# Optimization experiments

Measured on AMD Instinct MI355X. Metric: run time of the kernel, lower is better.

## Reference

```python
import jax, jax.numpy as jnp
import numpy as np

B, S, H, A, E = 64, 1024, 1024, 512, 512


def setup_inputs() -> dict:
    key = jax.random.key(0)
    ks = jax.random.split(key, 13)
    sc = 0.02
    return {
        "inputs": jax.random.normal(ks[0], (B, E), jnp.float32),
        "states": jax.random.normal(ks[1], (B, H), jnp.float32),
        "encoded": jax.random.normal(ks[2], (B, S, H), jnp.float32),
        "W_enc": jax.random.normal(ks[3], (H, A), jnp.float32) * sc,
        "b_enc": jax.random.normal(ks[4], (A,), jnp.float32) * sc,
        "W_dec": jax.random.normal(ks[5], (H, A), jnp.float32) * sc,
        "b_dec": jax.random.normal(ks[6], (A,), jnp.float32) * sc,
        "w_out": jax.random.normal(ks[7], (A,), jnp.float32) * sc,
        "b_out": jax.random.normal(ks[8], (1,), jnp.float32) * sc,
        "W_ih": jax.random.normal(ks[9], (E + H, 3 * H), jnp.float32) * sc,
        "b_ih": jax.random.normal(ks[10], (3 * H,), jnp.float32) * sc,
        "W_hh": jax.random.normal(ks[11], (H, 3 * H), jnp.float32) * sc,
        "b_hh": jax.random.normal(ks[12], (3 * H,), jnp.float32) * sc,
    }


def reference(inputs, states, encoded, W_enc, b_enc, W_dec, b_dec, w_out, b_out,
              W_ih, b_ih, W_hh, b_hh):
    # setup_memory: project encoder states once  [B,S,H] @ [H,A] -> [B,S,A]
    enc_proj = jnp.einsum('bsh,ha->bsa', encoded, W_enc) + b_enc
    # Bahdanau additive attention
    dec_proj = states @ W_dec + b_dec                       # [B,A]
    scores = jnp.einsum('bsa,a->bs', jnp.tanh(enc_proj + dec_proj[:, None, :]), w_out) + b_out[0]
    weights = jax.nn.softmax(scores, axis=1)                # [B,S]
    attention = jnp.einsum('bs,bsh->bh', weights, encoded)  # [B,H]
    x = jnp.concatenate([inputs, attention], axis=-1)       # [B,E+H]
    # GRUCell (PyTorch gate order r, z, n)
    gi = x @ W_ih + b_ih                                    # [B,3H]
    gh = states @ W_hh + b_hh                               # [B,3H]
    i_r, i_z, i_n = jnp.split(gi, 3, axis=-1)
    h_r, h_z, h_n = jnp.split(gh, 3, axis=-1)
    r = jax.nn.sigmoid(i_r + h_r)
    z = jax.nn.sigmoid(i_z + h_z)
    n = jnp.tanh(i_n + r * h_n)
    h_new = (1.0 - z) * n + z * states
    return h_new
```

## Files before the change

### kernel.cpp

```cpp
#include <hip/hip_runtime.h>
#include <hip/hip_bf16.h>


typedef __attribute__((ext_vector_type(8))) __bf16 bf16x8;
typedef __attribute__((ext_vector_type(4))) __bf16 bf16x4;
typedef __attribute__((ext_vector_type(4))) float f32x4;

__device__ __forceinline__ float fast_tanh(float x) {
  float xa = fminf(fmaxf(x, -15.f), 15.f);
  float e = __expf(2.f * xa);
  return (e - 1.f) / (e + 1.f);
}

#define GLOAD16(G, L)                                                              \
  __builtin_amdgcn_global_load_lds(                                                \
      (const __attribute__((address_space(1))) unsigned int*)(const void*)(G),     \
      (__attribute__((address_space(3))) unsigned int*)(void*)(L), 16, 0, 0)

__global__ __launch_bounds__(256) void wenc_t_kernel(const float* __restrict__ W,
                                                     __bf16* __restrict__ Wt) {
  __shared__ float tile[32][33];
  int k0 = blockIdx.x * 32, a0 = blockIdx.y * 32;
  int tid = threadIdx.x;
  int r = tid >> 3, c4 = (tid & 7) * 4;
  f32x4 v = *(const f32x4*)(W + (long)(k0 + r) * 512 + a0 + c4);
  tile[r][c4 + 0] = v.x; tile[r][c4 + 1] = v.y;
  tile[r][c4 + 2] = v.z; tile[r][c4 + 3] = v.w;
  __syncthreads();
  int a = tid >> 3, k4 = (tid & 7) * 4;
  bf16x4 o = { (__bf16)tile[k4 + 0][a], (__bf16)tile[k4 + 1][a],
               (__bf16)tile[k4 + 2][a], (__bf16)tile[k4 + 3][a] };
  *(bf16x4*)(Wt + (long)(a0 + a) * 1024 + k0 + k4) = o;
}

__global__ __launch_bounds__(256) void dec_proj_kernel(
    const float* __restrict__ states, const float* __restrict__ W_dec,
    const float* __restrict__ b_enc, const float* __restrict__ b_dec,
    float* __restrict__ addv) {
  int b = blockIdx.x, tid = threadIdx.x;
  int a = blockIdx.y * 256 + tid;
  __shared__ float sl[1024];
  for (int i = tid; i < 1024; i += 256) sl[i] = states[b * 1024 + i];
  __syncthreads();
  float c0 = 0.f, c1 = 0.f, c2 = 0.f, c3 = 0.f;
#pragma unroll 4
  for (int i = 0; i < 256; ++i) {
    c0 += sl[i]         * W_dec[(i)        * 512 + a];
    c1 += sl[i + 256]   * W_dec[(i + 256)  * 512 + a];
    c2 += sl[i + 512]   * W_dec[(i + 512)  * 512 + a];
    c3 += sl[i + 768]   * W_dec[(i + 768)  * 512 + a];
  }
  addv[b * 512 + a] = c0 + c1 + c2 + c3 + b_enc[a] + b_dec[a];
}

__global__ __launch_bounds__(256, 3) void enc_score_kernel(
    const float* __restrict__ encoded,
    const __bf16* __restrict__ Wt,
    const float* __restrict__ addv,
    const float* __restrict__ w_out,
    float* __restrict__ psc)
{
  __shared__ __attribute__((aligned(16))) char smem[50176];
  float* red = (float*)(smem + 49152);

  const int d = blockIdx.x;
  const int xcd = d & 7;
  const int slot = d >> 3;
  const int bn = slot & 3;
  const int bm = ((slot >> 2) << 3) | xcd;

  const int tid = threadIdx.x;
  const int lane = tid & 63;
  const int wid = tid >> 6;
  const int wr = wid >> 1;
  const int wc = wid & 1;
  const int lr = lane & 15;
  const int lkb = lane >> 4;

  const long row0 = (long)bm * 128;
  const int col0 = bn * 128;

  const int aslot = (tid & 7) ^ ((tid >> 3) & 7);
  const char* gA = (const char*)encoded + (row0 + (tid >> 3)) * 4096 + (aslot << 4);
  const int bslot = (tid & 3) ^ ((tid >> 3) & 3);
  const char* gB = (const char*)Wt + (long)(col0 + (tid >> 2)) * 2048 + (bslot << 4);
  const int ldsW = wid * 1024;

  const int aoff0 = ((2 * lkb) ^ (lr & 7)) << 4;
  const int aoff1 = ((2 * lkb + 1) ^ (lr & 7)) << 4;
  const int boff = (lkb ^ ((lr >> 1) & 3)) << 4;
  const int aRowB = (wr * 64 + lr) * 128;
  const int bColB = (wc * 64 + lr) * 64;

  f32x4 acc[4][4];
#pragma unroll
  for (int m = 0; m < 4; ++m)
#pragma unroll
    for (int n = 0; n < 4; ++n) acc[m][n] = (f32x4){0.f, 0.f, 0.f, 0.f};

#define STAGE(BUF, KT) do {                                                        \
    _Pragma("unroll") for (int _i = 0; _i < 4; ++_i)                               \
      GLOAD16(gA + (long)_i * 131072 + (KT) * 128,                                 \
              smem + (BUF) * 16384 + _i * 4096 + ldsW);                            \
    _Pragma("unroll") for (int _i = 0; _i < 2; ++_i)                               \
      GLOAD16(gB + (long)_i * 131072 + (KT) * 64,                                  \
              smem + 32768 + (BUF) * 8192 + _i * 4096 + ldsW);                     \
  } while (0)

#define COMPUTE(BUF) do {                                                          \
    const char* _Ab = smem + (BUF) * 16384;                                        \
    const char* _Bb = smem + 32768 + (BUF) * 8192;                                 \
    bf16x8 _af[4], _bv[4];                                                         \
    _Pragma("unroll") for (int _m = 0; _m < 4; ++_m) {                             \
      f32x4 _lo = *(const f32x4*)(_Ab + aRowB + _m * 2048 + aoff0);                \
      f32x4 _hi = *(const f32x4*)(_Ab + aRowB + _m * 2048 + aoff1);                \
      _Pragma("unroll") for (int _j = 0; _j < 4; ++_j) {                           \
        _af[_m][_j] = (__bf16)_lo[_j]; _af[_m][4 + _j] = (__bf16)_hi[_j];          \
      }                                                                            \
    }                                                                              \
    _Pragma("unroll") for (int _n = 0; _n < 4; ++_n)                               \
      _bv[_n] = *(const bf16x8*)(_Bb + bColB + _n * 1024 + boff);                  \
    _Pragma("unroll") for (int _m = 0; _m < 4; ++_m)                               \
      _Pragma("unroll") for (int _n = 0; _n < 4; ++_n)                             \
        acc[_m][_n] =                                                              \
            __builtin_amdgcn_mfma_f32_16x16x32_bf16(_af[_m], _bv[_n], acc[_m][_n], 0, 0, 0); \
  } while (0)

  STAGE(0, 0);
  __syncthreads();
  int buf = 0;
  for (int kt = 0; kt < 32; ++kt) {
    if (kt < 31) STAGE(buf ^ 1, kt + 1);
    COMPUTE(buf);
    __syncthreads();
    buf ^= 1;
  }

#undef STAGE
#undef COMPUTE

  const int b = bm >> 3;
  const float* addvb = addv + b * 512;
  float rowsum[4][4];
#pragma unroll
  for (int m = 0; m < 4; ++m)
#pragma unroll
    for (int reg = 0; reg < 4; ++reg) rowsum[m][reg] = 0.f;

#pragma unroll
  for (int m = 0; m < 4; ++m) {
#pragma unroll
    for (int n = 0; n < 4; ++n) {
      int col = col0 + wc * 64 + n * 16 + lr;
      float av = addvb[col];
      float wo = w_out[col];
#pragma unroll
      for (int reg = 0; reg < 4; ++reg)
        rowsum[m][reg] += fast_tanh(acc[m][n][reg] + av) * wo;
    }
  }
#pragma unroll
  for (int m = 0; m < 4; ++m)
#pragma unroll
    for (int reg = 0; reg < 4; ++reg) {
      float v = rowsum[m][reg];
      v += __shfl_xor(v, 1, 64);
      v += __shfl_xor(v, 2, 64);
      v += __shfl_xor(v, 4, 64);
      v += __shfl_xor(v, 8, 64);
      rowsum[m][reg] = v;
    }
  if (lr == 0) {
#pragma unroll
    for (int m = 0; m < 4; ++m)
#pragma unroll
      for (int reg = 0; reg < 4; ++reg)
        red[(wr * 64 + m * 16 + lkb * 4 + reg) * 2 + wc] = rowsum[m][reg];
  }
  __syncthreads();
  if (tid < 128)
    psc[(long)bn * 65536 + row0 + tid] = red[tid * 2] + red[tid * 2 + 1];
}

__global__ __launch_bounds__(256) void softmax_kernel(const float* __restrict__ psc,
                                                      float* __restrict__ wts) {
  int b = blockIdx.x, tid = threadIdx.x;
  __shared__ float sred[8];
  float sc[4];
  float mx = -1e30f;
#pragma unroll
  for (int i = 0; i < 4; ++i) {
    long r = (long)b * 1024 + tid + i * 256;
    sc[i] = psc[r] + psc[65536 + r] + psc[2 * 65536 + r] + psc[3 * 65536 + r];
    mx = fmaxf(mx, sc[i]);
  }
  for (int off = 1; off < 64; off <<= 1) mx = fmaxf(mx, __shfl_xor(mx, off, 64));
  if ((tid & 63) == 0) sred[tid >> 6] = mx;
  __syncthreads();
  mx = fmaxf(fmaxf(sred[0], sred[1]), fmaxf(sred[2], sred[3]));
  float e[4], sum = 0.f;
#pragma unroll
  for (int i = 0; i < 4; ++i) {
    e[i] = __expf(sc[i] - mx);
    sum += e[i];
  }
  for (int off = 1; off < 64; off <<= 1) sum += __shfl_xor(sum, off, 64);
  if ((tid & 63) == 0) sred[4 + (tid >> 6)] = sum;
  __syncthreads();
  sum = sred[4] + sred[5] + sred[6] + sred[7];
  float inv = 1.f / sum;
#pragma unroll
  for (int i = 0; i < 4; ++i) wts[(long)b * 1024 + tid + i * 256] = e[i] * inv;
}

__global__ __launch_bounds__(256) void att_part_kernel(const float* __restrict__ encoded,
                                                       const float* __restrict__ wts,
                                                       float* __restrict__ attp) {
  int chunk = blockIdx.x;
  int b = blockIdx.y;
  int tid = threadIdx.x;
  f32x4 a0 = (f32x4){0.f, 0.f, 0.f, 0.f};
  f32x4 a1 = a0, a2 = a0, a3 = a0;
  const float* base = encoded + ((long)b * 1024 + chunk * 64) * 1024 + tid * 4;
  const float* w = wts + b * 1024 + chunk * 64;
#pragma unroll 4
  for (int s = 0; s < 64; s += 4) {
    f32x4 v0 = *(const f32x4*)(base + (long)(s + 0) * 1024);
    f32x4 v1 = *(const f32x4*)(base + (long)(s + 1) * 1024);
    f32x4 v2 = *(const f32x4*)(base + (long)(s + 2) * 1024);
    f32x4 v3 = *(const f32x4*)(base + (long)(s + 3) * 1024);
    a0 += v0 * w[s]; a1 += v1 * w[s + 1]; a2 += v2 * w[s + 2]; a3 += v3 * w[s + 3];
  }
  *(f32x4*)(attp + ((long)(b * 16 + chunk)) * 1024 + tid * 4) = (a0 + a1) + (a2 + a3);
}

__global__ __launch_bounds__(256) void xcat_kernel(const float* __restrict__ inputs,
                                                   const float* __restrict__ attp,
                                                   float* __restrict__ xcat) {
  int b = blockIdx.y;
  int k = blockIdx.x * 256 + threadIdx.x;
  float v;
  if (k < 512) {
    v = inputs[b * 512 + k];
  } else {
    int h = k - 512;
    v = 0.f;
#pragma unroll
    for (int c = 0; c < 16; ++c) v += attp[((long)(b * 16 + c)) * 1024 + h];
  }
  xcat[(long)b * 1536 + k] = v;
}

__global__ __launch_bounds__(512) void gru_gemv_kernel(
    const float* __restrict__ xcat, const float* __restrict__ states,
    const float* __restrict__ W_ih, const float* __restrict__ b_ih,
    const float* __restrict__ W_hh, const float* __restrict__ b_hh,
    float* __restrict__ gi, float* __restrict__ gh) {
  __shared__ float sx[12288];
  const int dd = blockIdx.x;
  const int xcd = dd & 7;
  const int n = dd >> 3;
  const int cgrp = xcd + 8 * (n >> 3);
  const int bg = n & 7;
  const int tid = threadIdx.x;
  const int lcol = tid & 255;
  const int bsel = (tid >> 8) * 4;

  if (cgrp < 12) {
    const int col = cgrp * 256 + lcol;
    const float* xb = xcat + (long)bg * 8 * 1536;
    for (int i = tid; i < 3072; i += 512) ((f32x4*)sx)[i] = ((const f32x4*)xb)[i];
    __syncthreads();
    float a0 = b_ih[col], a1 = a0, a2 = a0, a3 = a0;
    const float* x0 = sx + (bsel + 0) * 1536;
    const float* x1 = sx + (bsel + 1) * 1536;
    const float* x2 = sx + (bsel + 2) * 1536;
    const float* x3 = sx + (bsel + 3) * 1536;
    for (int k = 0; k < 1536; k += 4) {
      f32x4 v0 = *(const f32x4*)(x0 + k);
      f32x4 v1 = *(const f32x4*)(x1 + k);
      f32x4 v2 = *(const f32x4*)(x2 + k);
      f32x4 v3 = *(const f32x4*)(x3 + k);
#pragma unroll
      for (int j = 0; j < 4; ++j) {
        float w = W_ih[(long)(k + j) * 3072 + col];
        a0 += v0[j] * w; a1 += v1[j] * w; a2 += v2[j] * w; a3 += v3[j] * w;
      }
    }
    long o = (long)(bg * 8 + bsel) * 3072 + col;
    gi[o] = a0; gi[o + 3072] = a1; gi[o + 6144] = a2; gi[o + 9216] = a3;
  } else {
    const int col = (cgrp - 12) * 256 + lcol;
    const float* sb = states + (long)bg * 8 * 1024;
    for (int i = tid; i < 2048; i += 512) ((f32x4*)sx)[i] = ((const f32x4*)sb)[i];
    __syncthreads();
    float a0 = b_hh[col], a1 = a0, a2 = a0, a3 = a0;
    const float* x0 = sx + (bsel + 0) * 1024;
    const float* x1 = sx + (bsel + 1) * 1024;
    const float* x2 = sx + (bsel + 2) * 1024;
    const float* x3 = sx + (bsel + 3) * 1024;
    for (int k = 0; k < 1024; k += 4) {
      f32x4 v0 = *(const f32x4*)(x0 + k);
      f32x4 v1 = *(const f32x4*)(x1 + k);
      f32x4 v2 = *(const f32x4*)(x2 + k);
      f32x4 v3 = *(const f32x4*)(x3 + k);
#pragma unroll
      for (int j = 0; j < 4; ++j) {
        float w = W_hh[(long)(k + j) * 3072 + col];
        a0 += v0[j] * w; a1 += v1[j] * w; a2 += v2[j] * w; a3 += v3[j] * w;
      }
    }
    long o = (long)(bg * 8 + bsel) * 3072 + col;
    gh[o] = a0; gh[o + 3072] = a1; gh[o + 6144] = a2; gh[o + 9216] = a3;
  }
}

__global__ __launch_bounds__(256) void gate_kernel(const float* __restrict__ gi,
                                                   const float* __restrict__ gh,
                                                   const float* __restrict__ states,
                                                   float* __restrict__ out) {
  int b = blockIdx.y;
  int j = blockIdx.x * 256 + threadIdx.x;
  long o = (long)b * 3072;
  float ir = gi[o + j], hr = gh[o + j];
  float iz = gi[o + 1024 + j], hz = gh[o + 1024 + j];
  float in_ = gi[o + 2048 + j], hn = gh[o + 2048 + j];
  float r = 1.f / (1.f + __expf(-(ir + hr)));
  float z = 1.f / (1.f + __expf(-(iz + hz)));
  float n = fast_tanh(in_ + r * hn);
  out[(long)b * 1024 + j] = (1.f - z) * n + z * states[(long)b * 1024 + j];
}

extern "C" void kernel_launch(void* const* d_in, const int* in_sizes, int n_in,
                              void* d_out, int out_size, void* d_ws, size_t ws_size,
                              hipStream_t stream) {
  const float* inputs  = (const float*)d_in[0];
  const float* states  = (const float*)d_in[1];
  const float* encoded = (const float*)d_in[2];
  const float* W_enc   = (const float*)d_in[3];
  const float* b_enc   = (const float*)d_in[4];
  const float* W_dec   = (const float*)d_in[5];
  const float* b_dec   = (const float*)d_in[6];
  const float* w_out   = (const float*)d_in[7];
  const float* W_ih    = (const float*)d_in[9];
  const float* b_ih    = (const float*)d_in[10];
  const float* W_hh    = (const float*)d_in[11];
  const float* b_hh    = (const float*)d_in[12];
  float* out = (float*)d_out;
  float* ws = (float*)d_ws;

  float* addv = ws;
  float* psc  = ws + 32768;
  float* wts  = ws + 294912;
  float* attp = ws + 360448;
  float* xcat = ws + 1409024;
  float* gi   = ws + 1507328;
  float* gh   = ws + 1703936;
  __bf16* Wt  = (__bf16*)(ws + 1900544);

  wenc_t_kernel<<<dim3(32, 16), 256, 0, stream>>>(W_enc, Wt);

  dim3 gA(64, 2);
  dec_proj_kernel<<<gA, 256, 0, stream>>>(states, W_dec, b_enc, b_dec, addv);

  enc_score_kernel<<<2048, 256, 0, stream>>>(encoded, Wt, addv, w_out, psc);

  softmax_kernel<<<64, 256, 0, stream>>>(psc, wts);

  dim3 gD(16, 64);
  att_part_kernel<<<gD, 256, 0, stream>>>(encoded, wts, attp);

  dim3 gE(6, 64);
  xcat_kernel<<<gE, 256, 0, stream>>>(inputs, attp, xcat);

  gru_gemv_kernel<<<192, 512, 0, stream>>>(xcat, states, W_ih, b_ih, W_hh, b_hh, gi, gh);

  dim3 gG(4, 64);
  gate_kernel<<<gG, 256, 0, stream>>>(gi, gh, states, out);
}
```

Baseline: 333.6 us.

## Pre-convert encoder states to bf16 in workspace for score GEMM and attention

Adds a pass that converts the whole fp32 encoded tensor to bf16 in workspace, used only when the workspace is large enough. The score GEMM then loads bf16 tiles straight into LDS with a smaller footprint and no in-loop fp32-to-bf16 conversion, and the attention-weighted sum reads the bf16 copy. The aim is to cut conversion ALU work and LDS traffic in the MFMA loop, and halve the bytes read by both consumers. In exchange, the extra pass reads the full fp32 tensor and writes a bf16 copy, so total memory traffic may rise. Attention values also lose precision. The original fp32 kernels remain as a fallback.

```diff
diff --git a/kernel.cpp b/kernel.cpp
--- a/kernel.cpp
+++ b/kernel.cpp
@@ -16,6 +16,23 @@
   __builtin_amdgcn_global_load_lds(                                                \
       (const __attribute__((address_space(1))) unsigned int*)(const void*)(G),     \
       (__attribute__((address_space(3))) unsigned int*)(void*)(L), 16, 0, 0)
+
+__global__ __launch_bounds__(256) void conv_kernel(const float* __restrict__ in,
+                                                   __bf16* __restrict__ out, long n16) {
+  long stride = (long)gridDim.x * 256;
+  for (long i = (long)blockIdx.x * 256 + threadIdx.x; i < n16; i += stride) {
+    const f32x4* p = (const f32x4*)(in + i * 16);
+    f32x4 v0 = p[0], v1 = p[1], v2 = p[2], v3 = p[3];
+    bf16x8 o0, o1;
+#pragma unroll
+    for (int j = 0; j < 4; ++j) {
+      o0[j] = (__bf16)v0[j]; o0[4 + j] = (__bf16)v1[j];
+      o1[j] = (__bf16)v2[j]; o1[4 + j] = (__bf16)v3[j];
+    }
+    *(bf16x8*)(out + i * 16) = o0;
+    *(bf16x8*)(out + i * 16 + 8) = o1;
+  }
+}
 
 __global__ __launch_bounds__(256) void wenc_t_kernel(const float* __restrict__ W,
                                                      __bf16* __restrict__ Wt) {
@@ -54,14 +71,14 @@
 }
 
 __global__ __launch_bounds__(256, 3) void enc_score_kernel(
-    const float* __restrict__ encoded,
+    const __bf16* __restrict__ encB,
     const __bf16* __restrict__ Wt,
     const float* __restrict__ addv,
     const float* __restrict__ w_out,
     float* __restrict__ psc)
 {
-  __shared__ __attribute__((aligned(16))) char smem[50176];
-  float* red = (float*)(smem + 49152);
+  __shared__ __attribute__((aligned(16))) char smem[33792];
+  float* red = (float*)(smem + 32768);
 
   const int d = blockIdx.x;
   const int xcd = d & 7;
@@ -80,24 +97,132 @@
   const long row0 = (long)bm * 128;
   const int col0 = bn * 128;
 
+  const int srow = tid >> 2;
+  const int sk8 = (tid & 3) ^ ((srow >> 1) & 3);
+  const __bf16* gA = encB + (row0 + srow) * 1024 + sk8 * 8;
+  const __bf16* gB = Wt + (long)(col0 + srow) * 1024 + sk8 * 8;
+  const int ldsW = wid * 1024;
+
+  const int foff = (lkb ^ ((lr >> 1) & 3)) << 4;
+  const int aRowB = (wr * 64 + lr) * 64;
+  const int bColB = (wc * 64 + lr) * 64;
+
+  f32x4 acc[4][4];
+#pragma unroll
+  for (int m = 0; m < 4; ++m)
+#pragma unroll
+    for (int n = 0; n < 4; ++n) acc[m][n] = (f32x4){0.f, 0.f, 0.f, 0.f};
+
+#define STAGE(BUF, KT) do {                                                        \
+    GLOAD16(gA + (KT) * 32,           smem + (BUF) * 8192 + ldsW);                 \
+    GLOAD16(gA + (KT) * 32 + 65536,   smem + (BUF) * 8192 + 4096 + ldsW);          \
+    GLOAD16(gB + (KT) * 32,           smem + 16384 + (BUF) * 8192 + ldsW);         \
+    GLOAD16(gB + (KT) * 32 + 65536,   smem + 16384 + (BUF) * 8192 + 4096 + ldsW);  \
+  } while (0)
+
+#define COMPUTE(BUF) do {                                                          \
+    const char* _Ab = smem + (BUF) * 8192;                                         \
+    const char* _Bb = smem + 16384 + (BUF) * 8192;                                 \
+    bf16x8 _af[4], _bv[4];                                                         \
+    _Pragma("unroll") for (int _m = 0; _m < 4; ++_m)                               \
+      _af[_m] = *(const bf16x8*)(_Ab + aRowB + _m * 1024 + foff);                  \
+    _Pragma("unroll") for (int _n = 0; _n < 4; ++_n)                               \
+      _bv[_n] = *(const bf16x8*)(_Bb + bColB + _n * 1024 + foff);                  \
+    _Pragma("unroll") for (int _m = 0; _m < 4; ++_m)                               \
+      _Pragma("unroll") for (int _n = 0; _n < 4; ++_n)                             \
+        acc[_m][_n] =                                                              \
+            __builtin_amdgcn_mfma_f32_16x16x32_bf16(_af[_m], _bv[_n], acc[_m][_n], 0, 0, 0); \
+  } while (0)
+
+  STAGE(0, 0);
+  __syncthreads();
+  int buf = 0;
+  for (int kt = 0; kt < 32; ++kt) {
+    if (kt < 31) STAGE(buf ^ 1, kt + 1);
+    COMPUTE(buf);
+    __syncthreads();
+    buf ^= 1;
+  }
+
+#undef STAGE
+#undef COMPUTE
+
+  const int b = bm >> 3;
+  const float* addvb = addv + b * 512;
+  float rowsum[4][4];
+#pragma unroll
+  for (int m = 0; m < 4; ++m)
+#pragma unroll
+    for (int reg = 0; reg < 4; ++reg) rowsum[m][reg] = 0.f;
+
+#pragma unroll
+  for (int m = 0; m < 4; ++m) {
+#pragma unroll
+    for (int n = 0; n < 4; ++n) {
+      int col = col0 + wc * 64 + n * 16 + lr;
+      float av = addvb[col];
+      float wo = w_out[col];
+#pragma unroll
+      for (int reg = 0; reg < 4; ++reg)
+        rowsum[m][reg] += fast_tanh(acc[m][n][reg] + av) * wo;
+    }
+  }
+#pragma unroll
+  for (int m = 0; m < 4; ++m)
+#pragma unroll
+    for (int reg = 0; reg < 4; ++reg) {
+      float v = rowsum[m][reg];
+      v += __shfl_xor(v, 1, 64);
+      v += __shfl_xor(v, 2, 64);
+      v += __shfl_xor(v, 4, 64);
+      v += __shfl_xor(v, 8, 64);
+      rowsum[m][reg] = v;
+    }
+  if (lr == 0) {
+#pragma unroll
+    for (int m = 0; m < 4; ++m)
+#pragma unroll
+      for (int reg = 0; reg < 4; ++reg)
+        red[(wr * 64 + m * 16 + lkb * 4 + reg) * 2 + wc] = rowsum[m][reg];
+  }
+  __syncthreads();
+  if (tid < 128)
+    psc[(long)bn * 65536 + row0 + tid] = red[tid * 2] + red[tid * 2 + 1];
+}
+
+__global__ __launch_bounds__(256, 3) void enc_score_f32_kernel(
+    const float* __restrict__ encoded, const __bf16* __restrict__ Wt,
+    const float* __restrict__ addv, const float* __restrict__ w_out,
+    float* __restrict__ psc) {
+  __shared__ __attribute__((aligned(16))) char smem[50176];
+  float* red = (float*)(smem + 49152);
+  const int d = blockIdx.x;
+  const int xcd = d & 7;
+  const int slot = d >> 3;
+  const int bn = slot & 3;
+  const int bm = ((slot >> 2) << 3) | xcd;
+  const int tid = threadIdx.x;
+  const int lane = tid & 63;
+  const int wid = tid >> 6;
+  const int wr = wid >> 1, wc = wid & 1;
+  const int lr = lane & 15, lkb = lane >> 4;
+  const long row0 = (long)bm * 128;
+  const int col0 = bn * 128;
   const int aslot = (tid & 7) ^ ((tid >> 3) & 7);
   const char* gA = (const char*)encoded + (row0 + (tid >> 3)) * 4096 + (aslot << 4);
   const int bslot = (tid & 3) ^ ((tid >> 3) & 3);
   const char* gB = (const char*)Wt + (long)(col0 + (tid >> 2)) * 2048 + (bslot << 4);
   const int ldsW = wid * 1024;
-
   const int aoff0 = ((2 * lkb) ^ (lr & 7)) << 4;
   const int aoff1 = ((2 * lkb + 1) ^ (lr & 7)) << 4;
   const int boff = (lkb ^ ((lr >> 1) & 3)) << 4;
   const int aRowB = (wr * 64 + lr) * 128;
   const int bColB = (wc * 64 + lr) * 64;
-
   f32x4 acc[4][4];
 #pragma unroll
   for (int m = 0; m < 4; ++m)
 #pragma unroll
     for (int n = 0; n < 4; ++n) acc[m][n] = (f32x4){0.f, 0.f, 0.f, 0.f};
-
 #define STAGE(BUF, KT) do {                                                        \
     _Pragma("unroll") for (int _i = 0; _i < 4; ++_i)                               \
       GLOAD16(gA + (long)_i * 131072 + (KT) * 128,                                 \
@@ -106,7 +231,6 @@
       GLOAD16(gB + (long)_i * 131072 + (KT) * 64,                                  \
               smem + 32768 + (BUF) * 8192 + _i * 4096 + ldsW);                     \
   } while (0)
-
 #define COMPUTE(BUF) do {                                                          \
     const char* _Ab = smem + (BUF) * 16384;                                        \
     const char* _Bb = smem + 32768 + (BUF) * 8192;                                 \
@@ -125,7 +249,6 @@
         acc[_m][_n] =                                                              \
             __builtin_amdgcn_mfma_f32_16x16x32_bf16(_af[_m], _bv[_n], acc[_m][_n], 0, 0, 0); \
   } while (0)
-
   STAGE(0, 0);
   __syncthreads();
   int buf = 0;
@@ -135,10 +258,8 @@
     __syncthreads();
     buf ^= 1;
   }
-
 #undef STAGE
 #undef COMPUTE
-
   const int b = bm >> 3;
   const float* addvb = addv + b * 512;
   float rowsum[4][4];
@@ -146,7 +267,6 @@
   for (int m = 0; m < 4; ++m)
 #pragma unroll
     for (int reg = 0; reg < 4; ++reg) rowsum[m][reg] = 0.f;
-
 #pragma unroll
   for (int m = 0; m < 4; ++m) {
 #pragma unroll
@@ -211,6 +331,33 @@
   float inv = 1.f / sum;
 #pragma unroll
   for (int i = 0; i < 4; ++i) wts[(long)b * 1024 + tid + i * 256] = e[i] * inv;
+}
+
+__global__ __launch_bounds__(128) void att_part_bf16_kernel(const __bf16* __restrict__ encB,
+                                                            const float* __restrict__ wts,
+                                                            float* __restrict__ attp) {
+  int chunk = blockIdx.x;
+  int b = blockIdx.y;
+  int tid = threadIdx.x;
+  const __bf16* base = encB + ((long)b * 1024 + chunk * 64) * 1024 + tid * 8;
+  const float* w = wts + b * 1024 + chunk * 64;
+  float a0[8], a1[8];
+#pragma unroll
+  for (int j = 0; j < 8; ++j) { a0[j] = 0.f; a1[j] = 0.f; }
+#pragma unroll 4
+  for (int s = 0; s < 64; s += 2) {
+    bf16x8 v0 = *(const bf16x8*)(base + (long)s * 1024);
+    bf16x8 v1 = *(const bf16x8*)(base + (long)(s + 1) * 1024);
+    float w0 = w[s], w1 = w[s + 1];
+#pragma unroll
+    for (int j = 0; j < 8; ++j) {
+      a0[j] += (float)v0[j] * w0;
+      a1[j] += (float)v1[j] * w1;
+    }
+  }
+  float* o = attp + ((long)(b * 16 + chunk)) * 1024 + tid * 8;
+#pragma unroll
+  for (int j = 0; j < 8; ++j) o[j] = a0[j] + a1[j];
 }
 
 __global__ __launch_bounds__(256) void att_part_kernel(const float* __restrict__ encoded,
@@ -349,26 +496,42 @@
   float* out = (float*)d_out;
   float* ws = (float*)d_ws;
 
-  float* addv = ws;
-  float* psc  = ws + 32768;
-  float* wts  = ws + 294912;
-  float* attp = ws + 360448;
-  float* xcat = ws + 1409024;
-  float* gi   = ws + 1507328;
-  float* gh   = ws + 1703936;
-  __bf16* Wt  = (__bf16*)(ws + 1900544);
+  const long ENC_ELEMS = 64L * 1024 * 1024;
+  const long ENCB_FLOATS = ENC_ELEMS / 2;
+  const long OTHERS_FLOATS = 2162688;
+  const bool big = ws_size >= (size_t)(ENCB_FLOATS + OTHERS_FLOATS) * 4;
+
+  __bf16* encB = (__bf16*)ws;
+  float* base = big ? ws + ENCB_FLOATS : ws;
+
+  float* addv = base;
+  float* psc  = base + 32768;
+  float* wts  = base + 294912;
+  float* attp = base + 360448;
+  float* xcat = base + 1409024;
+  float* gi   = base + 1507328;
+  float* gh   = base + 1703936;
+  __bf16* Wt  = (__bf16*)(base + 1900544);
+
+  if (big) conv_kernel<<<4096, 256, 0, stream>>>(encoded, encB, ENC_ELEMS / 16);
 
   wenc_t_kernel<<<dim3(32, 16), 256, 0, stream>>>(W_enc, Wt);
 
   dim3 gA(64, 2);
   dec_proj_kernel<<<gA, 256, 0, stream>>>(states, W_dec, b_enc, b_dec, addv);
 
-  enc_score_kernel<<<2048, 256, 0, stream>>>(encoded, Wt, addv, w_out, psc);
+  if (big)
+    enc_score_kernel<<<2048, 256, 0, stream>>>(encB, Wt, addv, w_out, psc);
+  else
+    enc_score_f32_kernel<<<2048, 256, 0, stream>>>(encoded, Wt, addv, w_out, psc);
 
   softmax_kernel<<<64, 256, 0, stream>>>(psc, wts);
 
   dim3 gD(16, 64);
-  att_part_kernel<<<gD, 256, 0, stream>>>(encoded, wts, attp);
+  if (big)
+    att_part_bf16_kernel<<<gD, 128, 0, stream>>>(encB, wts, attp);
+  else
+    att_part_kernel<<<gD, 256, 0, stream>>>(encoded, wts, attp);
 
   dim3 gE(6, 64);
   xcat_kernel<<<gE, 256, 0, stream>>>(inputs, attp, xcat);
```

After: 349.2 us. 1.05x slower.

## Pre-convert encoder states to bf16 and retile scoring GEMM with triple buffering

Applied to the files above, without the earlier changes.

Adds a conversion pass that writes a bf16 copy of the encoder states into workspace. The scoring GEMM and the attention-weighted sum then read that halved-size copy instead of fp32, which also removes the per-tile fp32-to-bf16 conversion inside the MFMA loop. The scoring GEMM grows to 256x256 tiles with 512 threads, so each row block is re-read by fewer column blocks. It also moves to a three-stage LDS pipeline with explicit waitcnt, barriers and setprio. In exchange it adds an extra full read and write pass over the encoder tensor, uses more LDS and registers per block, and lowers the precision of the attention accumulation inputs to bf16.

```diff
diff --git a/kernel.cpp b/kernel.cpp
--- a/kernel.cpp
+++ b/kernel.cpp
@@ -16,6 +16,23 @@
   __builtin_amdgcn_global_load_lds(                                                \
       (const __attribute__((address_space(1))) unsigned int*)(const void*)(G),     \
       (__attribute__((address_space(3))) unsigned int*)(void*)(L), 16, 0, 0)
+
+__global__ __launch_bounds__(256) void conv_kernel(const float* __restrict__ in,
+                                                   __bf16* __restrict__ out, long n16) {
+  long stride = (long)gridDim.x * 256;
+  for (long i = (long)blockIdx.x * 256 + threadIdx.x; i < n16; i += stride) {
+    const f32x4* p = (const f32x4*)(in + i * 16);
+    f32x4 v0 = p[0], v1 = p[1], v2 = p[2], v3 = p[3];
+    bf16x8 o0, o1;
+#pragma unroll
+    for (int j = 0; j < 4; ++j) {
+      o0[j] = (__bf16)v0[j]; o0[4 + j] = (__bf16)v1[j];
+      o1[j] = (__bf16)v2[j]; o1[4 + j] = (__bf16)v3[j];
+    }
+    *(bf16x8*)(out + i * 16) = o0;
+    *(bf16x8*)(out + i * 16 + 8) = o1;
+  }
+}
 
 __global__ __launch_bounds__(256) void wenc_t_kernel(const float* __restrict__ W,
                                                      __bf16* __restrict__ Wt) {
@@ -53,102 +70,120 @@
   addv[b * 512 + a] = c0 + c1 + c2 + c3 + b_enc[a] + b_dec[a];
 }
 
-__global__ __launch_bounds__(256, 3) void enc_score_kernel(
-    const float* __restrict__ encoded,
+__global__ __launch_bounds__(512, 2) void enc_score_kernel(
+    const __bf16* __restrict__ encB,
     const __bf16* __restrict__ Wt,
     const float* __restrict__ addv,
     const float* __restrict__ w_out,
     float* __restrict__ psc)
 {
-  __shared__ __attribute__((aligned(16))) char smem[50176];
-  float* red = (float*)(smem + 49152);
+  __shared__ __attribute__((aligned(16))) char smem[102400];
+  float* red = (float*)(smem + 98304);
 
   const int d = blockIdx.x;
   const int xcd = d & 7;
   const int slot = d >> 3;
-  const int bn = slot & 3;
-  const int bm = ((slot >> 2) << 3) | xcd;
+  const int bn = slot & 1;
+  const int bm = ((slot >> 1) << 3) | xcd;
 
   const int tid = threadIdx.x;
   const int lane = tid & 63;
   const int wid = tid >> 6;
-  const int wr = wid >> 1;
-  const int wc = wid & 1;
+  const int wr = wid >> 2;
+  const int wc = wid & 3;
   const int lr = lane & 15;
   const int lkb = lane >> 4;
 
-  const long row0 = (long)bm * 128;
-  const int col0 = bn * 128;
-
-  const int aslot = (tid & 7) ^ ((tid >> 3) & 7);
-  const char* gA = (const char*)encoded + (row0 + (tid >> 3)) * 4096 + (aslot << 4);
-  const int bslot = (tid & 3) ^ ((tid >> 3) & 3);
-  const char* gB = (const char*)Wt + (long)(col0 + (tid >> 2)) * 2048 + (bslot << 4);
+  const long row0 = (long)bm * 256;
+  const int col0 = bn * 256;
+
+  const int sk8 = (tid & 3) ^ ((tid >> 3) & 3);
+  const __bf16* gA = encB + (row0 + (tid >> 2)) * 1024 + sk8 * 8;
+  const __bf16* gB = Wt + (long)(col0 + (tid >> 2)) * 1024 + sk8 * 8;
   const int ldsW = wid * 1024;
 
-  const int aoff0 = ((2 * lkb) ^ (lr & 7)) << 4;
-  const int aoff1 = ((2 * lkb + 1) ^ (lr & 7)) << 4;
-  const int boff = (lkb ^ ((lr >> 1) & 3)) << 4;
-  const int aRowB = (wr * 64 + lr) * 128;
+  const int foff = (lkb ^ ((lr >> 1) & 3)) << 4;
+  const int aRowB = (wr * 128 + lr) * 64;
   const int bColB = (wc * 64 + lr) * 64;
 
-  f32x4 acc[4][4];
-#pragma unroll
-  for (int m = 0; m < 4; ++m)
+  f32x4 acc[8][4];
+#pragma unroll
+  for (int m = 0; m < 8; ++m)
 #pragma unroll
     for (int n = 0; n < 4; ++n) acc[m][n] = (f32x4){0.f, 0.f, 0.f, 0.f};
 
-#define STAGE(BUF, KT) do {                                                        \
-    _Pragma("unroll") for (int _i = 0; _i < 4; ++_i)                               \
-      GLOAD16(gA + (long)_i * 131072 + (KT) * 128,                                 \
-              smem + (BUF) * 16384 + _i * 4096 + ldsW);                            \
-    _Pragma("unroll") for (int _i = 0; _i < 2; ++_i)                               \
-      GLOAD16(gB + (long)_i * 131072 + (KT) * 64,                                  \
-              smem + 32768 + (BUF) * 8192 + _i * 4096 + ldsW);                     \
+#define STAGE(SBUF, KT) do {                                                       \
+    const __bf16* _a = gA + (KT) * 32;                                             \
+    const __bf16* _b = gB + (KT) * 32;                                             \
+    GLOAD16(_a,          smem + (SBUF) * 16384 + ldsW);                            \
+    GLOAD16(_a + 131072, smem + (SBUF) * 16384 + 8192 + ldsW);                     \
+    GLOAD16(_b,          smem + 49152 + (SBUF) * 16384 + ldsW);                    \
+    GLOAD16(_b + 131072, smem + 49152 + (SBUF) * 16384 + 8192 + ldsW);             \
+    __builtin_amdgcn_sched_barrier(0);                                             \
   } while (0)
 
-#define COMPUTE(BUF) do {                                                          \
-    const char* _Ab = smem + (BUF) * 16384;                                        \
-    const char* _Bb = smem + 32768 + (BUF) * 8192;                                 \
-    bf16x8 _af[4], _bv[4];                                                         \
-    _Pragma("unroll") for (int _m = 0; _m < 4; ++_m) {                             \
-      f32x4 _lo = *(const f32x4*)(_Ab + aRowB + _m * 2048 + aoff0);                \
-      f32x4 _hi = *(const f32x4*)(_Ab + aRowB + _m * 2048 + aoff1);                \
-      _Pragma("unroll") for (int _j = 0; _j < 4; ++_j) {                           \
-        _af[_m][_j] = (__bf16)_lo[_j]; _af[_m][4 + _j] = (__bf16)_hi[_j];          \
-      }                                                                            \
-    }                                                                              \
+#define COMPUTE(CBUF) do {                                                         \
+    const char* _Ab = smem + (CBUF) * 16384;                                       \
+    const char* _Bb = smem + 49152 + (CBUF) * 16384;                               \
+    bf16x8 _af[8], _bv[4];                                                         \
+    _Pragma("unroll") for (int _m = 0; _m < 8; ++_m)                               \
+      _af[_m] = *(const bf16x8*)(_Ab + aRowB + _m * 1024 + foff);                  \
     _Pragma("unroll") for (int _n = 0; _n < 4; ++_n)                               \
-      _bv[_n] = *(const bf16x8*)(_Bb + bColB + _n * 1024 + boff);                  \
-    _Pragma("unroll") for (int _m = 0; _m < 4; ++_m)                               \
+      _bv[_n] = *(const bf16x8*)(_Bb + bColB + _n * 1024 + foff);                  \
+    __builtin_amdgcn_s_setprio(1);                                                 \
+    _Pragma("unroll") for (int _m = 0; _m < 8; ++_m)                               \
       _Pragma("unroll") for (int _n = 0; _n < 4; ++_n)                             \
         acc[_m][_n] =                                                              \
             __builtin_amdgcn_mfma_f32_16x16x32_bf16(_af[_m], _bv[_n], acc[_m][_n], 0, 0, 0); \
+    __builtin_amdgcn_s_setprio(0);                                                 \
   } while (0)
 
+#define ITER(KT, CBUF, SBUF) do {                                                  \
+    asm volatile("s_waitcnt vmcnt(4)" ::: "memory");                               \
+    __builtin_amdgcn_sched_barrier(0);                                             \
+    __builtin_amdgcn_s_barrier();                                                  \
+    __builtin_amdgcn_sched_barrier(0);                                             \
+    COMPUTE(CBUF);                                                                 \
+    asm volatile("s_waitcnt lgkmcnt(0)" ::: "memory");                             \
+    __builtin_amdgcn_sched_barrier(0);                                             \
+    __builtin_amdgcn_s_barrier();                                                  \
+    __builtin_amdgcn_sched_barrier(0);                                             \
+    STAGE(SBUF, (KT) + 2);                                                         \
+  } while (0)
+
   STAGE(0, 0);
-  __syncthreads();
-  int buf = 0;
-  for (int kt = 0; kt < 32; ++kt) {
-    if (kt < 31) STAGE(buf ^ 1, kt + 1);
-    COMPUTE(buf);
-    __syncthreads();
-    buf ^= 1;
-  }
+  STAGE(1, 1);
+
+  for (int k3 = 0; k3 < 30; k3 += 3) {
+    ITER(k3 + 0, 0, 2);
+    ITER(k3 + 1, 1, 0);
+    ITER(k3 + 2, 2, 1);
+  }
+  asm volatile("s_waitcnt vmcnt(4)" ::: "memory");
+  __builtin_amdgcn_sched_barrier(0);
+  __builtin_amdgcn_s_barrier();
+  __builtin_amdgcn_sched_barrier(0);
+  COMPUTE(0);
+  asm volatile("s_waitcnt vmcnt(0)" ::: "memory");
+  __builtin_amdgcn_sched_barrier(0);
+  __builtin_amdgcn_s_barrier();
+  __builtin_amdgcn_sched_barrier(0);
+  COMPUTE(1);
 
 #undef STAGE
 #undef COMPUTE
-
-  const int b = bm >> 3;
+#undef ITER
+
+  const int b = bm >> 2;
   const float* addvb = addv + b * 512;
-  float rowsum[4][4];
-#pragma unroll
-  for (int m = 0; m < 4; ++m)
+  float rowsum[8][4];
+#pragma unroll
+  for (int m = 0; m < 8; ++m)
 #pragma unroll
     for (int reg = 0; reg < 4; ++reg) rowsum[m][reg] = 0.f;
 
 #pragma unroll
-  for (int m = 0; m < 4; ++m) {
+  for (int m = 0; m < 8; ++m) {
 #pragma unroll
     for (int n = 0; n < 4; ++n) {
       int col = col0 + wc * 64 + n * 16 + lr;
@@ -160,7 +195,7 @@
     }
   }
 #pragma unroll
-  for (int m = 0; m < 4; ++m)
+  for (int m = 0; m < 8; ++m)
 #pragma unroll
     for (int reg = 0; reg < 4; ++reg) {
       float v = rowsum[m][reg];
@@ -170,16 +205,18 @@
       v += __shfl_xor(v, 8, 64);
       rowsum[m][reg] = v;
     }
+  __syncthreads();
   if (lr == 0) {
 #pragma unroll
-    for (int m = 0; m < 4; ++m)
+    for (int m = 0; m < 8; ++m)
 #pragma unroll
       for (int reg = 0; reg < 4; ++reg)
-        red[(wr * 64 + m * 16 + lkb * 4 + reg) * 2 + wc] = rowsum[m][reg];
-  }
-  __syncthreads();
-  if (tid < 128)
-    psc[(long)bn * 65536 + row0 + tid] = red[tid * 2] + red[tid * 2 + 1];
+        red[(wr * 128 + m * 16 + lkb * 4 + reg) * 4 + wc] = rowsum[m][reg];
+  }
+  __syncthreads();
+  if (tid < 256)
+    psc[(long)bn * 65536 + row0 + tid] =
+        red[tid * 4] + red[tid * 4 + 1] + red[tid * 4 + 2] + red[tid * 4 + 3];
 }
 
 __global__ __launch_bounds__(256) void softmax_kernel(const float* __restrict__ psc,
@@ -191,7 +228,7 @@
 #pragma unroll
   for (int i = 0; i < 4; ++i) {
     long r = (long)b * 1024 + tid + i * 256;
-    sc[i] = psc[r] + psc[65536 + r] + psc[2 * 65536 + r] + psc[3 * 65536 + r];
+    sc[i] = psc[r] + psc[65536 + r];
     mx = fmaxf(mx, sc[i]);
   }
   for (int off = 1; off < 64; off <<= 1) mx = fmaxf(mx, __shfl_xor(mx, off, 64));
@@ -213,25 +250,31 @@
   for (int i = 0; i < 4; ++i) wts[(long)b * 1024 + tid + i * 256] = e[i] * inv;
 }
 
-__global__ __launch_bounds__(256) void att_part_kernel(const float* __restrict__ encoded,
-                                                       const float* __restrict__ wts,
-                                                       float* __restrict__ attp) {
+__global__ __launch_bounds__(128) void att_part_bf16_kernel(const __bf16* __restrict__ encB,
+                                                            const float* __restrict__ wts,
+                                                            float* __restrict__ attp) {
   int chunk = blockIdx.x;
   int b = blockIdx.y;
   int tid = threadIdx.x;
-  f32x4 a0 = (f32x4){0.f, 0.f, 0.f, 0.f};
-  f32x4 a1 = a0, a2 = a0, a3 = a0;
-  const float* base = encoded + ((long)b * 1024 + chunk * 64) * 1024 + tid * 4;
+  const __bf16* base = encB + ((long)b * 1024 + chunk * 64) * 1024 + tid * 8;
   const float* w = wts + b * 1024 + chunk * 64;
+  float a0[8], a1[8];
+#pragma unroll
+  for (int j = 0; j < 8; ++j) { a0[j] = 0.f; a1[j] = 0.f; }
 #pragma unroll 4
-  for (int s = 0; s < 64; s += 4) {
-    f32x4 v0 = *(const f32x4*)(base + (long)(s + 0) * 1024);
-    f32x4 v1 = *(const f32x4*)(base + (long)(s + 1) * 1024);
-    f32x4 v2 = *(const f32x4*)(base + (long)(s + 2) * 1024);
-    f32x4 v3 = *(const f32x4*)(base + (long)(s + 3) * 1024);
-    a0 += v0 * w[s]; a1 += v1 * w[s + 1]; a2 += v2 * w[s + 2]; a3 += v3 * w[s + 3];
-  }
-  *(f32x4*)(attp + ((long)(b * 16 + chunk)) * 1024 + tid * 4) = (a0 + a1) + (a2 + a3);
+  for (int s = 0; s < 64; s += 2) {
+    bf16x8 v0 = *(const bf16x8*)(base + (long)s * 1024);
+    bf16x8 v1 = *(const bf16x8*)(base + (long)(s + 1) * 1024);
+    float w0 = w[s], w1 = w[s + 1];
+#pragma unroll
+    for (int j = 0; j < 8; ++j) {
+      a0[j] += (float)v0[j] * w0;
+      a1[j] += (float)v1[j] * w1;
+    }
+  }
+  float* o = attp + ((long)(b * 16 + chunk)) * 1024 + tid * 8;
+#pragma unroll
+  for (int j = 0; j < 8; ++j) o[j] = a0[j] + a1[j];
 }
 
 __global__ __launch_bounds__(256) void xcat_kernel(const float* __restrict__ inputs,
@@ -349,26 +392,34 @@
   float* out = (float*)d_out;
   float* ws = (float*)d_ws;
 
-  float* addv = ws;
-  float* psc  = ws + 32768;
-  float* wts  = ws + 294912;
-  float* attp = ws + 360448;
-  float* xcat = ws + 1409024;
-  float* gi   = ws + 1507328;
-  float* gh   = ws + 1703936;
-  __bf16* Wt  = (__bf16*)(ws + 1900544);
+  const long ENC_ELEMS = 64L * 1024 * 1024;
+  const long ENCB_FLOATS = ENC_ELEMS / 2;
+
+  __bf16* encB = (__bf16*)ws;
+  float* base = ws + ENCB_FLOATS;
+
+  float* addv = base;
+  float* psc  = base + 32768;
+  float* wts  = base + 163840;
+  float* attp = base + 229376;
+  float* xcat = base + 1277952;
+  float* gi   = base + 1376256;
+  float* gh   = base + 1572864;
+  __bf16* Wt  = (__bf16*)(base + 1769472);
+
+  conv_kernel<<<4096, 256, 0, stream>>>(encoded, encB, ENC_ELEMS / 16);
 
   wenc_t_kernel<<<dim3(32, 16), 256, 0, stream>>>(W_enc, Wt);
 
   dim3 gA(64, 2);
   dec_proj_kernel<<<gA, 256, 0, stream>>>(states, W_dec, b_enc, b_dec, addv);
 
-  enc_score_kernel<<<2048, 256, 0, stream>>>(encoded, Wt, addv, w_out, psc);
+  enc_score_kernel<<<512, 512, 0, stream>>>(encB, Wt, addv, w_out, psc);
 
   softmax_kernel<<<64, 256, 0, stream>>>(psc, wts);
 
   dim3 gD(16, 64);
-  att_part_kernel<<<gD, 256, 0, stream>>>(encoded, wts, attp);
+  att_part_bf16_kernel<<<gD, 128, 0, stream>>>(encB, wts, attp);
 
   dim3 gE(6, 64);
   xcat_kernel<<<gE, 256, 0, stream>>>(inputs, attp, xcat);
```

Measured after the change: 341.4 us. 2.3% more time.
